# Performance work log

Measured on AMD Instinct MI355X. Metric: run time of the kernel, lower is better.

## Reference

```python
import jax, jax.numpy as jnp
import numpy as np

NUM_KEYS = 64

def setup_inputs() -> dict:
    key = jax.random.key(0)
    k1, k2 = jax.random.split(key)
    inputs = jax.random.randint(k1, (8, 4096, 1024), 0, NUM_KEYS, dtype=jnp.int32)
    # learned per-key bias (build() creates shape (num_keys,) for key_shape=[1])
    b = jax.random.normal(k2, (NUM_KEYS,), dtype=jnp.float32)
    # keys are sorted unique scalars (0..63), stored as float like the TF cast
    keys = jnp.arange(NUM_KEYS, dtype=jnp.float32)
    return {"inputs": inputs, "b": b, "keys": keys}


def reference(inputs, b, keys):
    # Original math: out = sum_k (inputs == keys[k]) * b[k], elementwise over inputs.
    # With unique sorted keys this is a gather: find the matching key index per
    # element and pick b there; elements matching no key contribute 0.
    # This avoids the O(num_keys * numel) broadcast blow-up of the TF graph.
    xf = inputs.astype(jnp.float32)
    K = keys.shape[0]
    idx = jnp.clip(jnp.searchsorted(keys, xf), 0, K - 1)  # [8,4096,1024]
    out = jnp.where(keys[idx] == xf, b[idx], jnp.float32(0.0))
    return out
```

## Files before the change

kernel.cpp:

```cpp
#include <hip/hip_runtime.h>

#define NKEYS 64
#define UNROLL 4

typedef int   __attribute__((ext_vector_type(4))) i32x4;
typedef float __attribute__((ext_vector_type(4))) f32x4;

__global__ __launch_bounds__(256) void sel_xform_kernel(
    const i32x4* __restrict__ in,
    const float* __restrict__ b,
    const float* __restrict__ keys,
    f32x4* __restrict__ out,
    int nvec, int slice, int ntail,
    const int* __restrict__ in_tail, float* __restrict__ out_tail)
{
    __shared__ float t[NKEYS];
    const int tid = threadIdx.x;
    if (tid < NKEYS) t[tid] = 0.0f;
    __syncthreads();
    if (tid < NKEYS) {
        const float kv = keys[tid];
        const int iv = (int)kv;
        if ((float)iv == kv && iv >= 0 && iv < NKEYS) {
            t[iv] = b[tid];
        }
    }
    __syncthreads();

    if (blockIdx.x == 0 && tid < ntail) {
        const int v = in_tail[tid];
        out_tail[tid] = ((unsigned)v < NKEYS) ? t[v] : 0.0f;
    }

    const int B = blockDim.x;
    const int begin = blockIdx.x * slice;
    if (begin >= nvec) return;
    const int end = (begin + slice < nvec) ? (begin + slice) : nvec;

    auto lut4 = [&](i32x4 v) -> f32x4 {
        const float rx = t[v.x & 63];
        const float ry = t[v.y & 63];
        const float rz = t[v.z & 63];
        const float rw = t[v.w & 63];
        f32x4 o;
        o.x = ((unsigned)v.x < NKEYS) ? rx : 0.0f;
        o.y = ((unsigned)v.y < NKEYS) ? ry : 0.0f;
        o.z = ((unsigned)v.z < NKEYS) ? rz : 0.0f;
        o.w = ((unsigned)v.w < NKEYS) ? rw : 0.0f;
        return o;
    };

    auto loadb = [&](int base, i32x4* dst, bool full) {
#pragma unroll
        for (int j = 0; j < UNROLL; ++j) {
            const int i = base + j * B + tid;
            if (full || i < end) dst[j] = __builtin_nontemporal_load(in + i);
            else                 dst[j] = i32x4{0, 0, 0, 0};
        }
    };
    auto storeb = [&](int base, const i32x4* v, bool full) {
#pragma unroll
        for (int j = 0; j < UNROLL; ++j) {
            const int i = base + j * B + tid;
            if (full || i < end)
                __builtin_nontemporal_store(lut4(v[j]), out + i);
        }
    };

    int base = begin;
    i32x4 cur[UNROLL];
    bool cur_full = (base + UNROLL * B) <= end;
    loadb(base, cur, cur_full);
    while (true) {
        const int nbase = base + UNROLL * B;
        const bool have_next = nbase < end;
        i32x4 nxt[UNROLL];
        bool nxt_full = false;
        if (have_next) {
            nxt_full = (nbase + UNROLL * B) <= end;
            loadb(nbase, nxt, nxt_full);
        }
        storeb(base, cur, cur_full);
        if (!have_next) break;
#pragma unroll
        for (int j = 0; j < UNROLL; ++j) cur[j] = nxt[j];
        cur_full = nxt_full;
        base = nbase;
    }
}

extern "C" void kernel_launch(void* const* d_in, const int* in_sizes, int n_in,
                              void* d_out, int out_size, void* d_ws, size_t ws_size,
                              hipStream_t stream) {
    const int*   x    = (const int*)d_in[0];
    const float* b    = (const float*)d_in[1];
    const float* keys = (const float*)d_in[2];
    float* out = (float*)d_out;

    const int n    = in_sizes[0];
    const int nvec = n >> 2;
    const int ntail = n & 3;

    const int block = 256;
    const int batch = block * UNROLL;

    int grid = (nvec + batch - 1) / batch;
    if (grid > 2048) grid = 2048;
    if (grid < 1) grid = 1;
    int slice = (nvec + grid - 1) / grid;
    slice = ((slice + batch - 1) / batch) * batch;
    grid = (nvec + slice - 1) / slice;

    sel_xform_kernel<<<grid, block, 0, stream>>>(
        (const i32x4*)x, b, keys, (f32x4*)out,
        nvec, slice, ntail, x + (nvec << 2), out + (nvec << 2));
}
```

Measured before the change: 227.0 us.

## Replace software-pipelined loop with simple unrolled batches and shrink grid

Drops the explicit double-buffered load/store pipeline and uses a plain loop that loads eight vectors and then stores eight per iteration, with a separate tail loop. UNROLL goes from 4 to 8 and the grid is capped at 512 blocks instead of 2048, so each block covers a larger contiguous slice. The aim is to cut register pressure and control overhead while keeping enough loads in flight. The cost is less cross-iteration overlap and fewer resident blocks to hide memory latency on a large-CU device.

```diff
diff --git a/kernel.cpp b/kernel.cpp
--- a/kernel.cpp
+++ b/kernel.cpp
@@ -1,7 +1,7 @@
 #include <hip/hip_runtime.h>
 
 #define NKEYS 64
-#define UNROLL 4
+#define UNROLL 8
 
 typedef int   __attribute__((ext_vector_type(4))) i32x4;
 typedef float __attribute__((ext_vector_type(4))) f32x4;
@@ -32,11 +32,6 @@
         out_tail[tid] = ((unsigned)v < NKEYS) ? t[v] : 0.0f;
     }
 
-    const int B = blockDim.x;
-    const int begin = blockIdx.x * slice;
-    if (begin >= nvec) return;
-    const int end = (begin + slice < nvec) ? (begin + slice) : nvec;
-
     auto lut4 = [&](i32x4 v) -> f32x4 {
         const float rx = t[v.x & 63];
         const float ry = t[v.y & 63];
@@ -50,42 +45,28 @@
         return o;
     };
 
-    auto loadb = [&](int base, i32x4* dst, bool full) {
-#pragma unroll
-        for (int j = 0; j < UNROLL; ++j) {
-            const int i = base + j * B + tid;
-            if (full || i < end) dst[j] = __builtin_nontemporal_load(in + i);
-            else                 dst[j] = i32x4{0, 0, 0, 0};
-        }
-    };
-    auto storeb = [&](int base, const i32x4* v, bool full) {
-#pragma unroll
-        for (int j = 0; j < UNROLL; ++j) {
-            const int i = base + j * B + tid;
-            if (full || i < end)
-                __builtin_nontemporal_store(lut4(v[j]), out + i);
-        }
-    };
+    const int B = blockDim.x;
+    const int batch = B * UNROLL;
+    const int begin = blockIdx.x * slice;
+    if (begin >= nvec) return;
+    const int end = (begin + slice < nvec) ? (begin + slice) : nvec;
 
     int base = begin;
-    i32x4 cur[UNROLL];
-    bool cur_full = (base + UNROLL * B) <= end;
-    loadb(base, cur, cur_full);
-    while (true) {
-        const int nbase = base + UNROLL * B;
-        const bool have_next = nbase < end;
-        i32x4 nxt[UNROLL];
-        bool nxt_full = false;
-        if (have_next) {
-            nxt_full = (nbase + UNROLL * B) <= end;
-            loadb(nbase, nxt, nxt_full);
+    for (; base + batch <= end; base += batch) {
+        i32x4 v[UNROLL];
+#pragma unroll
+        for (int j = 0; j < UNROLL; ++j)
+            v[j] = __builtin_nontemporal_load(in + base + j * B + tid);
+#pragma unroll
+        for (int j = 0; j < UNROLL; ++j)
+            __builtin_nontemporal_store(lut4(v[j]), out + base + j * B + tid);
+    }
+    for (; base < end; base += B) {
+        const int i = base + tid;
+        if (i < end) {
+            const i32x4 v = __builtin_nontemporal_load(in + i);
+            __builtin_nontemporal_store(lut4(v), out + i);
         }
-        storeb(base, cur, cur_full);
-        if (!have_next) break;
-#pragma unroll
-        for (int j = 0; j < UNROLL; ++j) cur[j] = nxt[j];
-        cur_full = nxt_full;
-        base = nbase;
     }
 }
 
@@ -104,8 +85,9 @@
     const int block = 256;
     const int batch = block * UNROLL;
 
-    int grid = (nvec + batch - 1) / batch;
-    if (grid > 2048) grid = 2048;
+    int grid = 512;
+    int maxg = (nvec + batch - 1) / batch;
+    if (grid > maxg) grid = maxg;
     if (grid < 1) grid = 1;
     int slice = (nvec + grid - 1) / grid;
     slice = ((slice + batch - 1) / batch) * batch;
```

After: 228.2 us. No clear change (+0.5%).
